# Optimization experiments

Measured on AMD Instinct MI355X. Metric: run time of the kernel, lower is better.

The kernel has to match this reference:

```python
import jax, jax.numpy as jnp
import numpy as np

B, N, T, C, H = 4, 1024, 32, 256, 8
LN_EPS = 1e-5


def setup_inputs() -> dict:
    key = jax.random.key(0)
    ks = jax.random.split(key, 10)
    BN = B * N
    x = jax.random.normal(ks[0], (BN, T, C), dtype=jnp.float32)
    # frame timestamps, sorted increasing, moderate scale so decay bias is meaningful
    timestamps = jnp.sort(jax.random.uniform(ks[1], (B, T), dtype=jnp.float32) * 64.0, axis=1)
    s = 0.02
    params = {
        'ln_gamma': jnp.ones((C,), jnp.float32),
        'ln_beta': jnp.zeros((C,), jnp.float32),
        'Wq': jax.random.normal(ks[2], (C, C), jnp.float32) * s,
        'bq': jnp.zeros((C,), jnp.float32),
        'Wk': jax.random.normal(ks[3], (C, C), jnp.float32) * s,
        'Wv': jax.random.normal(ks[4], (C, C), jnp.float32) * s,
        'Wg': jax.random.normal(ks[5], (C, C), jnp.float32) * s,
        # out_proj is zero-init in the module; use small random here so output is non-trivial
        'Wo': jax.random.normal(ks[6], (C, C), jnp.float32) * s,
        'log_lambda': jnp.linspace(np.log(0.004), np.log(0.7), H).astype(jnp.float32),
    }
    return {'x': x, 'timestamps': timestamps, 'n_spatial': N, **params}


def reference(x, timestamps, n_spatial, ln_gamma, ln_beta, Wq, bq, Wk, Wv, Wg, Wo, log_lambda):
    BN, T_, C_ = x.shape
    Bb = BN // n_spatial
    Hh = log_lambda.shape[0]
    d = C_ // Hh

    # LayerNorm
    mu = jnp.mean(x, axis=-1, keepdims=True)
    var = jnp.mean(jnp.square(x - mu), axis=-1, keepdims=True)
    h = (x - mu) * jax.lax.rsqrt(var + LN_EPS) * ln_gamma + ln_beta

    q = (h @ Wq.T + bq).reshape(BN, T_, Hh, d)
    k = (h @ Wk.T).reshape(BN, T_, Hh, d)
    v = (h @ Wv.T).reshape(BN, T_, Hh, d)
    g = jax.nn.sigmoid(h @ Wg.T)

    # temporal decay bias: (B, H, T, T), broadcast over spatial positions
    dt = jnp.abs(timestamps[:, :, None] - timestamps[:, None, :])  # (B,T,T)
    bias = -jnp.exp(log_lambda)[None, :, None, None] * dt[:, None, :, :]  # (B,H,T,T)

    scores = jnp.einsum('bthd,bshd->bhts', q.astype(jnp.float32), k.astype(jnp.float32))
    scores = scores / jnp.sqrt(jnp.float32(d))
    # broadcast bias instead of repeat_interleave: (B, N, H, T, T)
    scores = scores.reshape(Bb, n_spatial, Hh, T_, T_) + bias[:, None]
    attn = jax.nn.softmax(scores, axis=-1).reshape(BN, Hh, T_, T_)

    o = jnp.einsum('bhts,bshd->bthd', attn, v.astype(jnp.float32)).astype(v.dtype)
    o = o.reshape(BN, T_, C_)
    return x + (g * o) @ Wo.T
```

## Files before the change

### kernel.cpp

```cpp
#include <hip/hip_runtime.h>
#include <hip/hip_bf16.h>


typedef __attribute__((ext_vector_type(8))) short  s16x8;
typedef __attribute__((ext_vector_type(4))) float  f32x4;
typedef __attribute__((ext_vector_type(4))) unsigned short us16x4;

#define MFMA16(a, b, c) __builtin_amdgcn_mfma_f32_16x16x32_bf16((a), (b), (c), 0, 0, 0)

static __device__ __forceinline__ short f2bf(float f) {
  union { float f; unsigned u; } v; v.f = f;
  unsigned r = (v.u + 0x7FFFu + ((v.u >> 16) & 1u)) >> 16;
  return (short)r;
}

#define RS      528
#define VTS     80
#define LDS_H   0
#define LDS_Q   33792
#define LDS_K   67584
#define LDS_VT  101376
#define LDS_TS  142336
#define LDS_TOTAL 142464

#define WS_WQ   0
#define WS_WK   131072
#define WS_WV   262144
#define WS_WG   393216
#define WS_WO   524288
#define WS_LAM  655360
#define WS_NEED 655392

__global__ void prep_kernel(const float* __restrict__ Wq, const float* __restrict__ Wk,
                            const float* __restrict__ Wv, const float* __restrict__ Wg,
                            const float* __restrict__ Wo, const float* __restrict__ ll,
                            char* __restrict__ ws) {
  int tid = blockIdx.x * 256 + threadIdx.x;
  if (tid < 5 * 8192) {
    int m      = tid >> 13;
    int within = tid & 8191;
    int lane   = within & 63;
    int j = 16 * (within >> 9) + (lane & 15);
    int c = 32 * ((within >> 6) & 7) + 8 * (lane >> 4);
    const float* W = (m == 0) ? Wq : (m == 1) ? Wk : (m == 2) ? Wv : (m == 3) ? Wg : Wo;
    const float* src = W + j * 256 + c;
    s16x8 o;
#pragma unroll
    for (int i = 0; i < 8; ++i) o[i] = f2bf(src[i]);
    *(s16x8*)(ws + (size_t)tid * 16) = o;
  } else if (tid < 5 * 8192 + 8) {
    ((float*)(ws + WS_LAM))[tid - 40960] = __expf(ll[tid - 40960]);
  }
}

static __device__ __forceinline__ void gemm32(const char* lds, int aoff,
                                              const char* wsb, int w, int lane,
                                              f32x4 acc[4][2]) {
  const int l15 = lane & 15, l4 = lane >> 4;
  const s16x8* Bf = (const s16x8*)wsb + (2 * w * 8) * 64 + lane;
#pragma unroll
  for (int ks = 0; ks < 8; ++ks) {
    s16x8 a[4];
#pragma unroll
    for (int mt = 0; mt < 4; ++mt)
      a[mt] = *(const s16x8*)(lds + aoff + (16 * mt + l15) * RS + 64 * ks + 16 * l4);
#pragma unroll
    for (int nt = 0; nt < 2; ++nt) {
      s16x8 b = Bf[(nt * 8 + ks) * 64];
#pragma unroll
      for (int mt = 0; mt < 4; ++mt) acc[mt][nt] = MFMA16(a[mt], b, acc[mt][nt]);
    }
  }
}

__global__ __launch_bounds__(512, 2) void fused_kernel(
    const float* __restrict__ x, const float* __restrict__ tsg,
    const float* __restrict__ gamma, const float* __restrict__ beta,
    const float* __restrict__ bq, const char* __restrict__ ws,
    float* __restrict__ out) {
  extern __shared__ __align__(16) char lds[];
  const int tid = threadIdx.x;
  const int lane = tid & 63;
  const int w = tid >> 6;
  const int l15 = lane & 15, l4 = lane >> 4;
  const int blk = blockIdx.x;

  {
    const int r = tid >> 3;
    const int sub = tid & 7;
    const float* xr = x + ((size_t)blk * 64 + r) * 256 + sub * 32;
    float4 xv[8];
    float s = 0.f, s2 = 0.f;
#pragma unroll
    for (int u = 0; u < 8; ++u) {
      xv[u] = *(const float4*)(xr + 4 * u);
      s  += xv[u].x + xv[u].y + xv[u].z + xv[u].w;
      s2 += xv[u].x * xv[u].x + xv[u].y * xv[u].y + xv[u].z * xv[u].z + xv[u].w * xv[u].w;
    }
#pragma unroll
    for (int m = 1; m <= 4; m <<= 1) { s += __shfl_xor(s, m); s2 += __shfl_xor(s2, m); }
    float mu = s * (1.f / 256.f);
    float rstd = rsqrtf(s2 * (1.f / 256.f) - mu * mu + 1e-5f);
#pragma unroll
    for (int u = 0; u < 8; ++u) {
      int c = sub * 32 + 4 * u;
      float4 gv = *(const float4*)(gamma + c);
      float4 bv = *(const float4*)(beta + c);
      us16x4 hb;
      hb[0] = (unsigned short)f2bf((xv[u].x - mu) * rstd * gv.x + bv.x);
      hb[1] = (unsigned short)f2bf((xv[u].y - mu) * rstd * gv.y + bv.y);
      hb[2] = (unsigned short)f2bf((xv[u].z - mu) * rstd * gv.z + bv.z);
      hb[3] = (unsigned short)f2bf((xv[u].w - mu) * rstd * gv.w + bv.w);
      *(us16x4*)(lds + LDS_H + r * RS + 2 * c) = hb;
    }
    if (tid < 32) ((float*)(lds + LDS_TS))[tid] = tsg[(blk >> 9) * 32 + tid];
  }
  __syncthreads();

  float bqv0 = bq[32 * w + l15], bqv1 = bq[32 * w + 16 + l15];
  f32x4 acc[4][4][2];
#pragma unroll
  for (int gm = 0; gm < 4; ++gm)
#pragma unroll
    for (int mt = 0; mt < 4; ++mt)
#pragma unroll
      for (int nt = 0; nt < 2; ++nt) acc[gm][mt][nt] = (f32x4){0.f, 0.f, 0.f, 0.f};
  {
    const s16x8* Bq = (const s16x8*)(ws + WS_WQ) + (2 * w * 8) * 64 + lane;
    const s16x8* Bk = (const s16x8*)(ws + WS_WK) + (2 * w * 8) * 64 + lane;
    const s16x8* Bv = (const s16x8*)(ws + WS_WV) + (2 * w * 8) * 64 + lane;
    const s16x8* Bg = (const s16x8*)(ws + WS_WG) + (2 * w * 8) * 64 + lane;
#pragma unroll
    for (int ks = 0; ks < 8; ++ks) {
      s16x8 a[4];
#pragma unroll
      for (int mt = 0; mt < 4; ++mt)
        a[mt] = *(const s16x8*)(lds + LDS_H + (16 * mt + l15) * RS + 64 * ks + 16 * l4);
#pragma unroll
      for (int nt = 0; nt < 2; ++nt) {
        s16x8 b0 = Bq[(nt * 8 + ks) * 64];
        s16x8 b1 = Bk[(nt * 8 + ks) * 64];
        s16x8 b2 = Bv[(nt * 8 + ks) * 64];
        s16x8 b3 = Bg[(nt * 8 + ks) * 64];
#pragma unroll
        for (int mt = 0; mt < 4; ++mt) {
          acc[0][mt][nt] = MFMA16(a[mt], b0, acc[0][mt][nt]);
          acc[1][mt][nt] = MFMA16(a[mt], b1, acc[1][mt][nt]);
          acc[2][mt][nt] = MFMA16(a[mt], b2, acc[2][mt][nt]);
          acc[3][mt][nt] = MFMA16(a[mt], b3, acc[3][mt][nt]);
        }
      }
    }
  }
#pragma unroll
  for (int mt = 0; mt < 4; ++mt)
#pragma unroll
    for (int nt = 0; nt < 2; ++nt)
#pragma unroll
      for (int r = 0; r < 4; ++r) {
        int row = 16 * mt + 4 * l4 + r;
        int j = 32 * w + 16 * nt + l15;
        float qv = (acc[0][mt][nt][r] + (nt ? bqv1 : bqv0)) * 0.17677669529663687f;
        *(short*)(lds + LDS_Q + row * RS + 2 * j) = f2bf(qv);
        *(short*)(lds + LDS_K + row * RS + 2 * j) = f2bf(acc[1][mt][nt][r]);
        *(short*)(lds + LDS_VT + (row >> 5) * 20480 + j * VTS + 2 * (row & 31)) =
            f2bf(acc[2][mt][nt][r]);
        acc[3][mt][nt][r] = 1.f / (1.f + __expf(-acc[3][mt][nt][r]));
      }
  __syncthreads();

  const float lamh = ((const float*)(ws + WS_LAM))[w];
  const float* tsl = (const float*)(lds + LDS_TS);
  float tc0 = tsl[l15], tc1 = tsl[l15 + 16];
  float trow[8];
#pragma unroll
  for (int mt = 0; mt < 2; ++mt)
#pragma unroll
    for (int r = 0; r < 4; ++r) trow[mt * 4 + r] = tsl[4 * l4 + r + 16 * mt];

#pragma unroll
  for (int half = 0; half < 2; ++half) {
    const int rb = 32 * half;
    const f32x4 zf = {0.f, 0.f, 0.f, 0.f};
    s16x8 aq[2], bk[2];
#pragma unroll
    for (int mt = 0; mt < 2; ++mt)
      aq[mt] = *(const s16x8*)(lds + LDS_Q + (rb + 16 * mt + l15) * RS + 64 * w + 16 * l4);
#pragma unroll
    for (int nt = 0; nt < 2; ++nt)
      bk[nt] = *(const s16x8*)(lds + LDS_K + (rb + 16 * nt + l15) * RS + 64 * w + 16 * l4);
    f32x4 sc[2][2];
#pragma unroll
    for (int mt = 0; mt < 2; ++mt)
#pragma unroll
      for (int nt = 0; nt < 2; ++nt) sc[mt][nt] = MFMA16(aq[mt], bk[nt], zf);

#pragma unroll
    for (int mt = 0; mt < 2; ++mt)
#pragma unroll
      for (int r = 0; r < 4; ++r) {
        float a0 = sc[mt][0][r] - lamh * fabsf(trow[mt * 4 + r] - tc0);
        float a1 = sc[mt][1][r] - lamh * fabsf(trow[mt * 4 + r] - tc1);
        float m = fmaxf(a0, a1);
        m = fmaxf(m, __shfl_xor(m, 1)); m = fmaxf(m, __shfl_xor(m, 2));
        m = fmaxf(m, __shfl_xor(m, 4)); m = fmaxf(m, __shfl_xor(m, 8));
        float e0 = __expf(a0 - m), e1 = __expf(a1 - m);
        float sum = e0 + e1;
        sum += __shfl_xor(sum, 1); sum += __shfl_xor(sum, 2);
        sum += __shfl_xor(sum, 4); sum += __shfl_xor(sum, 8);
        float inv = 1.0f / sum;
        int t = 4 * l4 + r + 16 * mt;
        *(short*)(lds + w * 2560 + t * VTS + 2 * l15)        = f2bf(e0 * inv);
        *(short*)(lds + w * 2560 + t * VTS + 2 * (l15 + 16)) = f2bf(e1 * inv);
      }
    asm volatile("s_waitcnt lgkmcnt(0)" ::: "memory");

    s16x8 ap[2], bv[2];
#pragma unroll
    for (int mt = 0; mt < 2; ++mt)
      ap[mt] = *(const s16x8*)(lds + w * 2560 + (16 * mt + l15) * VTS + 16 * l4);
#pragma unroll
    for (int nd = 0; nd < 2; ++nd)
      bv[nd] = *(const s16x8*)(lds + LDS_VT + half * 20480 +
                               (32 * w + 16 * nd + l15) * VTS + 16 * l4);
#pragma unroll
    for (int mt = 0; mt < 2; ++mt)
#pragma unroll
      for (int nd = 0; nd < 2; ++nd) {
        f32x4 oa = MFMA16(ap[mt], bv[nd], zf);
#pragma unroll
        for (int r = 0; r < 4; ++r) {
          float go = oa[r] * acc[3][2 * half + mt][nd][r];
          int row = rb + 16 * mt + 4 * l4 + r;
          int j = 32 * w + 16 * nd + l15;
          *(short*)(lds + LDS_Q + row * RS + 2 * j) = f2bf(go);
        }
      }
    asm volatile("s_waitcnt lgkmcnt(0)" ::: "memory");
  }
  __syncthreads();

  {
    f32x4 facc[4][2];
#pragma unroll
    for (int mt = 0; mt < 4; ++mt)
#pragma unroll
      for (int nt = 0; nt < 2; ++nt) facc[mt][nt] = (f32x4){0.f, 0.f, 0.f, 0.f};
    gemm32(lds, LDS_Q, ws + WS_WO, w, lane, facc);
#pragma unroll
    for (int mt = 0; mt < 4; ++mt)
#pragma unroll
      for (int nt = 0; nt < 2; ++nt)
#pragma unroll
        for (int r = 0; r < 4; ++r) {
          int row = 16 * mt + 4 * l4 + r;
          int j = 32 * w + 16 * nt + l15;
          size_t gi = ((size_t)blk * 64 + row) * 256 + j;
          out[gi] = facc[mt][nt][r] + x[gi];
        }
  }
}

extern "C" void kernel_launch(void* const* d_in, const int* in_sizes, int n_in,
                              void* d_out, int out_size, void* d_ws, size_t ws_size,
                              hipStream_t stream) {
  const float* x     = (const float*)d_in[0];
  const float* ts    = (const float*)d_in[1];
  const float* gamma = (const float*)d_in[3];
  const float* beta  = (const float*)d_in[4];
  const float* Wq    = (const float*)d_in[5];
  const float* bq    = (const float*)d_in[6];
  const float* Wk    = (const float*)d_in[7];
  const float* Wv    = (const float*)d_in[8];
  const float* Wg    = (const float*)d_in[9];
  const float* Wo    = (const float*)d_in[10];
  const float* ll    = (const float*)d_in[11];
  char* ws   = (char*)d_ws;
  float* out = (float*)d_out;

  prep_kernel<<<161, 256, 0, stream>>>(Wq, Wk, Wv, Wg, Wo, ll, ws);

  (void)hipFuncSetAttribute((const void*)fused_kernel,
                            hipFuncAttributeMaxDynamicSharedMemorySize, LDS_TOTAL);
  fused_kernel<<<2048, 512, LDS_TOTAL, stream>>>(x, ts, gamma, beta, bq, ws, out);
}
```

Measured before the change: 460.9 us.

## Shrink LDS and registers: sequential per-projection GEMMs with per-wave attention zones

```diff
diff --git a/kernel.cpp b/kernel.cpp
--- a/kernel.cpp
+++ b/kernel.cpp
@@ -8,20 +8,26 @@
 
 #define MFMA16(a, b, c) __builtin_amdgcn_mfma_f32_16x16x32_bf16((a), (b), (c), 0, 0, 0)
 
-static __device__ __forceinline__ short f2bf(float f) {
+static __device__ __forceinline__ unsigned short f2bfu(float f) {
   union { float f; unsigned u; } v; v.f = f;
-  unsigned r = (v.u + 0x7FFFu + ((v.u >> 16) & 1u)) >> 16;
-  return (short)r;
+  return (unsigned short)((v.u + 0x7FFFu + ((v.u >> 16) & 1u)) >> 16);
+}
+static __device__ __forceinline__ float bf_lo(unsigned u) {
+  union { unsigned u; float f; } v; v.u = u << 16; return v.f;
+}
+static __device__ __forceinline__ float bf_hi(unsigned u) {
+  union { unsigned u; float f; } v; v.u = u & 0xFFFF0000u; return v.f;
 }
 
 #define RS      528
-#define VTS     80
-#define LDS_H   0
-#define LDS_Q   33792
-#define LDS_K   67584
-#define LDS_VT  101376
-#define LDS_TS  142336
-#define LDS_TOTAL 142464
+#define ZSTR    72
+#define ZQ      0
+#define ZV      2304
+#define ZONE    4736
+#define LDS_A   0
+#define LDS_TS  33792
+#define LDS_Z   33920
+#define LDS_TOTAL (LDS_Z + 8 * ZONE)
 
 #define WS_WQ   0
 #define WS_WK   131072
@@ -29,7 +35,6 @@
 #define WS_WG   393216
 #define WS_WO   524288
 #define WS_LAM  655360
-#define WS_NEED 655392
 
 __global__ void prep_kernel(const float* __restrict__ Wq, const float* __restrict__ Wk,
                             const float* __restrict__ Wv, const float* __restrict__ Wg,
@@ -46,24 +51,27 @@
     const float* src = W + j * 256 + c;
     s16x8 o;
 #pragma unroll
-    for (int i = 0; i < 8; ++i) o[i] = f2bf(src[i]);
+    for (int i = 0; i < 8; ++i) o[i] = (short)f2bfu(src[i]);
     *(s16x8*)(ws + (size_t)tid * 16) = o;
   } else if (tid < 5 * 8192 + 8) {
     ((float*)(ws + WS_LAM))[tid - 40960] = __expf(ll[tid - 40960]);
   }
 }
 
-static __device__ __forceinline__ void gemm32(const char* lds, int aoff,
-                                              const char* wsb, int w, int lane,
-                                              f32x4 acc[4][2]) {
+static __device__ __forceinline__ void gemm_h(const char* lds, const char* wmat,
+                                              int w, int lane, f32x4 acc[4][2]) {
   const int l15 = lane & 15, l4 = lane >> 4;
-  const s16x8* Bf = (const s16x8*)wsb + (2 * w * 8) * 64 + lane;
+#pragma unroll
+  for (int mt = 0; mt < 4; ++mt)
+#pragma unroll
+    for (int nt = 0; nt < 2; ++nt) acc[mt][nt] = (f32x4){0.f, 0.f, 0.f, 0.f};
+  const s16x8* Bf = (const s16x8*)wmat + 16 * w * 64 + lane;
 #pragma unroll
   for (int ks = 0; ks < 8; ++ks) {
     s16x8 a[4];
 #pragma unroll
     for (int mt = 0; mt < 4; ++mt)
-      a[mt] = *(const s16x8*)(lds + aoff + (16 * mt + l15) * RS + 64 * ks + 16 * l4);
+      a[mt] = *(const s16x8*)(lds + LDS_A + (16 * mt + l15) * RS + 64 * ks + 16 * l4);
 #pragma unroll
     for (int nt = 0; nt < 2; ++nt) {
       s16x8 b = Bf[(nt * 8 + ks) * 64];
@@ -73,7 +81,7 @@
   }
 }
 
-__global__ __launch_bounds__(512, 2) void fused_kernel(
+__global__ __launch_bounds__(512, 4) void fused_kernel(
     const float* __restrict__ x, const float* __restrict__ tsg,
     const float* __restrict__ gamma, const float* __restrict__ beta,
     const float* __restrict__ bq, const char* __restrict__ ws,
@@ -84,10 +92,10 @@
   const int w = tid >> 6;
   const int l15 = lane & 15, l4 = lane >> 4;
   const int blk = blockIdx.x;
+  char* zone = lds + LDS_Z + w * ZONE;
 
   {
-    const int r = tid >> 3;
-    const int sub = tid & 7;
+    const int r = tid >> 3, sub = tid & 7;
     const float* xr = x + ((size_t)blk * 64 + r) * 256 + sub * 32;
     float4 xv[8];
     float s = 0.f, s2 = 0.f;
@@ -107,146 +115,150 @@
       float4 gv = *(const float4*)(gamma + c);
       float4 bv = *(const float4*)(beta + c);
       us16x4 hb;
-      hb[0] = (unsigned short)f2bf((xv[u].x - mu) * rstd * gv.x + bv.x);
-      hb[1] = (unsigned short)f2bf((xv[u].y - mu) * rstd * gv.y + bv.y);
-      hb[2] = (unsigned short)f2bf((xv[u].z - mu) * rstd * gv.z + bv.z);
-      hb[3] = (unsigned short)f2bf((xv[u].w - mu) * rstd * gv.w + bv.w);
-      *(us16x4*)(lds + LDS_H + r * RS + 2 * c) = hb;
+      hb[0] = f2bfu((xv[u].x - mu) * rstd * gv.x + bv.x);
+      hb[1] = f2bfu((xv[u].y - mu) * rstd * gv.y + bv.y);
+      hb[2] = f2bfu((xv[u].z - mu) * rstd * gv.z + bv.z);
+      hb[3] = f2bfu((xv[u].w - mu) * rstd * gv.w + bv.w);
+      *(us16x4*)(lds + LDS_A + r * RS + 2 * c) = hb;
     }
     if (tid < 32) ((float*)(lds + LDS_TS))[tid] = tsg[(blk >> 9) * 32 + tid];
   }
   __syncthreads();
 
-  float bqv0 = bq[32 * w + l15], bqv1 = bq[32 * w + 16 + l15];
-  f32x4 acc[4][4][2];
-#pragma unroll
-  for (int gm = 0; gm < 4; ++gm)
+  f32x4 acc[4][2];
+  unsigned gpk[4][2][2], vpk[4][2][2];
+  s16x8 bk[2][2];
+
+  gemm_h(lds, ws + WS_WG, w, lane, acc);
+#pragma unroll
+  for (int mt = 0; mt < 4; ++mt)
+#pragma unroll
+    for (int nt = 0; nt < 2; ++nt)
+#pragma unroll
+      for (int rp = 0; rp < 2; ++rp) {
+        float lo = 1.f / (1.f + __expf(-acc[mt][nt][2 * rp]));
+        float hi = 1.f / (1.f + __expf(-acc[mt][nt][2 * rp + 1]));
+        gpk[mt][nt][rp] = (unsigned)f2bfu(lo) | ((unsigned)f2bfu(hi) << 16);
+      }
+
+  gemm_h(lds, ws + WS_WV, w, lane, acc);
+#pragma unroll
+  for (int mt = 0; mt < 4; ++mt)
+#pragma unroll
+    for (int nt = 0; nt < 2; ++nt)
+#pragma unroll
+      for (int rp = 0; rp < 2; ++rp)
+        vpk[mt][nt][rp] = (unsigned)f2bfu(acc[mt][nt][2 * rp]) |
+                          ((unsigned)f2bfu(acc[mt][nt][2 * rp + 1]) << 16);
+
+  gemm_h(lds, ws + WS_WK, w, lane, acc);
+#pragma unroll
+  for (int seq = 0; seq < 2; ++seq) {
+#pragma unroll
+    for (int mh = 0; mh < 2; ++mh)
+#pragma unroll
+      for (int nt = 0; nt < 2; ++nt)
+#pragma unroll
+        for (int r = 0; r < 4; ++r)
+          *(short*)(zone + ZQ + (16 * mh + 4 * l4 + r) * ZSTR + 2 * (16 * nt + l15)) =
+              (short)f2bfu(acc[2 * seq + mh][nt][r]);
+#pragma unroll
+    for (int nt = 0; nt < 2; ++nt)
+      bk[seq][nt] = *(const s16x8*)(zone + ZQ + (16 * nt + l15) * ZSTR + 16 * l4);
+  }
+
+  gemm_h(lds, ws + WS_WQ, w, lane, acc);
+  __syncthreads();
+
+  {
+    float bq0 = bq[32 * w + l15], bq1 = bq[32 * w + 16 + l15];
 #pragma unroll
     for (int mt = 0; mt < 4; ++mt)
 #pragma unroll
-      for (int nt = 0; nt < 2; ++nt) acc[gm][mt][nt] = (f32x4){0.f, 0.f, 0.f, 0.f};
-  {
-    const s16x8* Bq = (const s16x8*)(ws + WS_WQ) + (2 * w * 8) * 64 + lane;
-    const s16x8* Bk = (const s16x8*)(ws + WS_WK) + (2 * w * 8) * 64 + lane;
-    const s16x8* Bv = (const s16x8*)(ws + WS_WV) + (2 * w * 8) * 64 + lane;
-    const s16x8* Bg = (const s16x8*)(ws + WS_WG) + (2 * w * 8) * 64 + lane;
-#pragma unroll
-    for (int ks = 0; ks < 8; ++ks) {
-      s16x8 a[4];
-#pragma unroll
-      for (int mt = 0; mt < 4; ++mt)
-        a[mt] = *(const s16x8*)(lds + LDS_H + (16 * mt + l15) * RS + 64 * ks + 16 * l4);
-#pragma unroll
-      for (int nt = 0; nt < 2; ++nt) {
-        s16x8 b0 = Bq[(nt * 8 + ks) * 64];
-        s16x8 b1 = Bk[(nt * 8 + ks) * 64];
-        s16x8 b2 = Bv[(nt * 8 + ks) * 64];
-        s16x8 b3 = Bg[(nt * 8 + ks) * 64];
-#pragma unroll
-        for (int mt = 0; mt < 4; ++mt) {
-          acc[0][mt][nt] = MFMA16(a[mt], b0, acc[0][mt][nt]);
-          acc[1][mt][nt] = MFMA16(a[mt], b1, acc[1][mt][nt]);
-          acc[2][mt][nt] = MFMA16(a[mt], b2, acc[2][mt][nt]);
-          acc[3][mt][nt] = MFMA16(a[mt], b3, acc[3][mt][nt]);
-        }
-      }
-    }
-  }
-#pragma unroll
-  for (int mt = 0; mt < 4; ++mt)
-#pragma unroll
-    for (int nt = 0; nt < 2; ++nt)
-#pragma unroll
-      for (int r = 0; r < 4; ++r) {
-        int row = 16 * mt + 4 * l4 + r;
-        int j = 32 * w + 16 * nt + l15;
-        float qv = (acc[0][mt][nt][r] + (nt ? bqv1 : bqv0)) * 0.17677669529663687f;
-        *(short*)(lds + LDS_Q + row * RS + 2 * j) = f2bf(qv);
-        *(short*)(lds + LDS_K + row * RS + 2 * j) = f2bf(acc[1][mt][nt][r]);
-        *(short*)(lds + LDS_VT + (row >> 5) * 20480 + j * VTS + 2 * (row & 31)) =
-            f2bf(acc[2][mt][nt][r]);
-        acc[3][mt][nt][r] = 1.f / (1.f + __expf(-acc[3][mt][nt][r]));
-      }
-  __syncthreads();
+      for (int nt = 0; nt < 2; ++nt)
+#pragma unroll
+        for (int r = 0; r < 4; ++r)
+          acc[mt][nt][r] = (acc[mt][nt][r] + (nt ? bq1 : bq0)) * 0.17677669529663687f;
+  }
 
   const float lamh = ((const float*)(ws + WS_LAM))[w];
   const float* tsl = (const float*)(lds + LDS_TS);
-  float tc0 = tsl[l15], tc1 = tsl[l15 + 16];
+  const float tc0 = tsl[l15], tc1 = tsl[l15 + 16];
   float trow[8];
 #pragma unroll
-  for (int mt = 0; mt < 2; ++mt)
-#pragma unroll
-    for (int r = 0; r < 4; ++r) trow[mt * 4 + r] = tsl[4 * l4 + r + 16 * mt];
-
-#pragma unroll
-  for (int half = 0; half < 2; ++half) {
-    const int rb = 32 * half;
-    const f32x4 zf = {0.f, 0.f, 0.f, 0.f};
-    s16x8 aq[2], bk[2];
-#pragma unroll
-    for (int mt = 0; mt < 2; ++mt)
-      aq[mt] = *(const s16x8*)(lds + LDS_Q + (rb + 16 * mt + l15) * RS + 64 * w + 16 * l4);
-#pragma unroll
-    for (int nt = 0; nt < 2; ++nt)
-      bk[nt] = *(const s16x8*)(lds + LDS_K + (rb + 16 * nt + l15) * RS + 64 * w + 16 * l4);
+  for (int mh = 0; mh < 2; ++mh)
+#pragma unroll
+    for (int r = 0; r < 4; ++r) trow[mh * 4 + r] = tsl[16 * mh + 4 * l4 + r];
+  const f32x4 zf = {0.f, 0.f, 0.f, 0.f};
+
+#pragma unroll
+  for (int seq = 0; seq < 2; ++seq) {
+#pragma unroll
+    for (int mh = 0; mh < 2; ++mh)
+#pragma unroll
+      for (int nt = 0; nt < 2; ++nt)
+#pragma unroll
+        for (int rp = 0; rp < 2; ++rp)
+          *(unsigned*)(zone + ZV + (16 * nt + l15) * ZSTR + 2 * (16 * mh + 4 * l4 + 2 * rp)) =
+              vpk[2 * seq + mh][nt][rp];
+#pragma unroll
+    for (int mh = 0; mh < 2; ++mh)
+#pragma unroll
+      for (int nt = 0; nt < 2; ++nt)
+#pragma unroll
+        for (int r = 0; r < 4; ++r)
+          *(short*)(zone + ZQ + (16 * mh + 4 * l4 + r) * ZSTR + 2 * (16 * nt + l15)) =
+              (short)f2bfu(acc[2 * seq + mh][nt][r]);
+    s16x8 aq0 = *(const s16x8*)(zone + ZQ + l15 * ZSTR + 16 * l4);
+    s16x8 aq1 = *(const s16x8*)(zone + ZQ + (16 + l15) * ZSTR + 16 * l4);
     f32x4 sc[2][2];
-#pragma unroll
-    for (int mt = 0; mt < 2; ++mt)
-#pragma unroll
-      for (int nt = 0; nt < 2; ++nt) sc[mt][nt] = MFMA16(aq[mt], bk[nt], zf);
-
-#pragma unroll
-    for (int mt = 0; mt < 2; ++mt)
+    sc[0][0] = MFMA16(aq0, bk[seq][0], zf);
+    sc[0][1] = MFMA16(aq0, bk[seq][1], zf);
+    sc[1][0] = MFMA16(aq1, bk[seq][0], zf);
+    sc[1][1] = MFMA16(aq1, bk[seq][1], zf);
+#pragma unroll
+    for (int mh = 0; mh < 2; ++mh)
 #pragma unroll
       for (int r = 0; r < 4; ++r) {
-        float a0 = sc[mt][0][r] - lamh * fabsf(trow[mt * 4 + r] - tc0);
-        float a1 = sc[mt][1][r] - lamh * fabsf(trow[mt * 4 + r] - tc1);
+        float tr = trow[mh * 4 + r];
+        float a0 = sc[mh][0][r] - lamh * fabsf(tr - tc0);
+        float a1 = sc[mh][1][r] - lamh * fabsf(tr - tc1);
         float m = fmaxf(a0, a1);
         m = fmaxf(m, __shfl_xor(m, 1)); m = fmaxf(m, __shfl_xor(m, 2));
         m = fmaxf(m, __shfl_xor(m, 4)); m = fmaxf(m, __shfl_xor(m, 8));
         float e0 = __expf(a0 - m), e1 = __expf(a1 - m);
-        float sum = e0 + e1;
-        sum += __shfl_xor(sum, 1); sum += __shfl_xor(sum, 2);
-        sum += __shfl_xor(sum, 4); sum += __shfl_xor(sum, 8);
-        float inv = 1.0f / sum;
-        int t = 4 * l4 + r + 16 * mt;
-        *(short*)(lds + w * 2560 + t * VTS + 2 * l15)        = f2bf(e0 * inv);
-        *(short*)(lds + w * 2560 + t * VTS + 2 * (l15 + 16)) = f2bf(e1 * inv);
+        float su = e0 + e1;
+        su += __shfl_xor(su, 1); su += __shfl_xor(su, 2);
+        su += __shfl_xor(su, 4); su += __shfl_xor(su, 8);
+        float inv = 1.0f / su;
+        int t = 16 * mh + 4 * l4 + r;
+        *(short*)(zone + ZQ + t * ZSTR + 2 * l15)        = (short)f2bfu(e0 * inv);
+        *(short*)(zone + ZQ + t * ZSTR + 2 * (l15 + 16)) = (short)f2bfu(e1 * inv);
       }
-    asm volatile("s_waitcnt lgkmcnt(0)" ::: "memory");
-
-    s16x8 ap[2], bv[2];
-#pragma unroll
-    for (int mt = 0; mt < 2; ++mt)
-      ap[mt] = *(const s16x8*)(lds + w * 2560 + (16 * mt + l15) * VTS + 16 * l4);
-#pragma unroll
-    for (int nd = 0; nd < 2; ++nd)
-      bv[nd] = *(const s16x8*)(lds + LDS_VT + half * 20480 +
-                               (32 * w + 16 * nd + l15) * VTS + 16 * l4);
-#pragma unroll
-    for (int mt = 0; mt < 2; ++mt)
+    s16x8 ap0 = *(const s16x8*)(zone + ZQ + l15 * ZSTR + 16 * l4);
+    s16x8 ap1 = *(const s16x8*)(zone + ZQ + (16 + l15) * ZSTR + 16 * l4);
+    s16x8 bv0 = *(const s16x8*)(zone + ZV + l15 * ZSTR + 16 * l4);
+    s16x8 bv1 = *(const s16x8*)(zone + ZV + (16 + l15) * ZSTR + 16 * l4);
+#pragma unroll
+    for (int mh = 0; mh < 2; ++mh)
 #pragma unroll
       for (int nd = 0; nd < 2; ++nd) {
-        f32x4 oa = MFMA16(ap[mt], bv[nd], zf);
+        f32x4 oa = MFMA16(mh ? ap1 : ap0, nd ? bv1 : bv0, zf);
 #pragma unroll
         for (int r = 0; r < 4; ++r) {
-          float go = oa[r] * acc[3][2 * half + mt][nd][r];
-          int row = rb + 16 * mt + 4 * l4 + r;
+          unsigned gu = gpk[2 * seq + mh][nd][r >> 1];
+          float gv = (r & 1) ? bf_hi(gu) : bf_lo(gu);
+          int row = 32 * seq + 16 * mh + 4 * l4 + r;
           int j = 32 * w + 16 * nd + l15;
-          *(short*)(lds + LDS_Q + row * RS + 2 * j) = f2bf(go);
+          *(short*)(lds + LDS_A + row * RS + 2 * j) = (short)f2bfu(oa[r] * gv);
         }
       }
-    asm volatile("s_waitcnt lgkmcnt(0)" ::: "memory");
   }
   __syncthreads();
 
   {
     f32x4 facc[4][2];
-#pragma unroll
-    for (int mt = 0; mt < 4; ++mt)
-#pragma unroll
-      for (int nt = 0; nt < 2; ++nt) facc[mt][nt] = (f32x4){0.f, 0.f, 0.f, 0.f};
-    gemm32(lds, LDS_Q, ws + WS_WO, w, lane, facc);
+    gemm_h(lds, ws + WS_WO, w, lane, facc);
 #pragma unroll
     for (int mt = 0; mt < 4; ++mt)
 #pragma unroll
```

New measurement: 624.3 us. 1.35x slower.
